# Optimization experiments

Measured on AMD Instinct MI355X. Metric: run time of the kernel, lower is better.

## Reference

```python
import jax, jax.numpy as jnp
import numpy as np

N_NODES = 50000
N_EDGES = 800000
IN_CH = 128
HID_CH = 128
OUT_CH = 64
N_GRAPHS = 256


def setup_inputs() -> dict:
    key = jax.random.key(0)
    k1, k2, k3, k4, k5, k6, k7 = jax.random.split(key, 7)
    x = jax.random.normal(k1, (N_NODES, IN_CH), dtype=jnp.float32)
    edge_index = jax.random.randint(k2, (2, N_EDGES), 0, N_NODES, dtype=jnp.int64)
    batch = jnp.sort(jax.random.randint(k3, (N_NODES,), 0, N_GRAPHS, dtype=jnp.int64))
    # GCNConv params (glorot-ish scale) and Linear params
    W1 = jax.random.normal(k4, (IN_CH, HID_CH), dtype=jnp.float32) / np.sqrt(IN_CH)
    b1 = jnp.zeros((HID_CH,), dtype=jnp.float32)
    W2 = jax.random.normal(k5, (HID_CH, OUT_CH), dtype=jnp.float32) / np.sqrt(HID_CH)
    b2 = jax.random.normal(k6, (OUT_CH,), dtype=jnp.float32) * 0.01
    return {"x": x, "edge_index": edge_index, "batch": batch,
            "W1": W1, "b1": b1, "W2": W2, "b2": b2}


def _gcn_conv(x, edge_index, W, b):
    # PyG GCNConv: add self loops, symmetric normalization, linear transform,
    # gather-scale-scatter aggregation, bias.
    n = x.shape[0]
    loop = jnp.arange(n, dtype=edge_index.dtype)
    src = jnp.concatenate([edge_index[0], loop])  # message sources
    dst = jnp.concatenate([edge_index[1], loop])  # aggregation targets
    deg = jax.ops.segment_sum(jnp.ones_like(dst, dtype=x.dtype), dst, num_segments=n)
    dinv = jnp.where(deg > 0, jax.lax.rsqrt(deg), 0.0)
    norm = dinv[src] * dinv[dst]                  # [E+N]
    h = x @ W                                     # [N, hid] transform first (in >= hid)
    msg = h[src] * norm[:, None]                  # [E+N, hid] gather + scale
    agg = jax.ops.segment_sum(msg, dst, num_segments=n)  # scatter-add
    return agg + b


def reference(x, edge_index, batch, W1, b1, W2, b2):
    h = _gcn_conv(x, edge_index, W1, b1)
    h = jax.nn.relu(h)
    # dropout is identity in eval mode
    pooled = jax.ops.segment_max(h, batch, num_segments=N_GRAPHS)  # global max pool
    pooled = jnp.where(jnp.isfinite(pooled), pooled, 0.0)          # empty graphs -> 0
    out = jax.nn.relu(pooled @ W2 + b2)
    return out
```

## Files before the change

### kernel.cpp

```cpp
#include <hip/hip_runtime.h>

#define NN 50000
#define NE 800000
#define NG 256
#define NB 256
#define BW 196
#define NBIN 200
#define EPB 4000
#define NGEMM 391
#define PAD 16
#define CAP 4608
#define WT_STRIDE 136

typedef __attribute__((ext_vector_type(8))) short bf16x8;
typedef __attribute__((ext_vector_type(4))) float f32x4;
typedef __attribute__((ext_vector_type(2))) float f32x2;

static __device__ __forceinline__ unsigned short f2b(float f) {
    unsigned int u = __float_as_uint(f);
    return (unsigned short)((u + 0x7FFFu + ((u >> 16) & 1u)) >> 16);
}
static __device__ __forceinline__ unsigned char f2e4m3(float f) {
    int p = __builtin_amdgcn_cvt_pk_fp8_f32(f, 0.f, 0, false);
    return (unsigned char)(p & 0xFF);
}

__global__ __launch_bounds__(256) void k_front(const float* __restrict__ x,
                                               const float* __restrict__ W,
                                               unsigned char* __restrict__ h8,
                                               const int* __restrict__ src,
                                               const int* __restrict__ dst,
                                               int* __restrict__ bcur,
                                               unsigned int* __restrict__ ebuf) {
    __shared__ unsigned short Ws[128 * WT_STRIDE];
    const int tid = threadIdx.x;

    if (blockIdx.x >= NGEMM) {
        int* lh = (int*)Ws;
        int* gb = lh + NB;
        int* lc = gb + NB;
        lh[tid] = 0; lc[tid] = 0;
        __syncthreads();
        int e0 = (blockIdx.x - NGEMM) * EPB;
        for (int i = e0 + tid; i < e0 + EPB; i += 256)
            atomicAdd(&lh[(unsigned)dst[i] / BW], 1);
        __syncthreads();
        if (lh[tid]) gb[tid] = tid * CAP + atomicAdd(&bcur[tid * PAD], lh[tid]);
        __syncthreads();
        for (int i = e0 + tid; i < e0 + EPB; i += 256) {
            int d = dst[i];
            int b = (unsigned)d / BW;
            int r = atomicAdd(&lc[b], 1);
            ebuf[gb[b] + r] = ((unsigned)(d - b * BW) << 17) | (unsigned)src[i];
        }
        return;
    }

#pragma unroll
    for (int p = 0; p < 64; ++p) {
        int g = p * 256 + tid;
        int k = g >> 7, n = g & 127;
        Ws[n * WT_STRIDE + k] = f2b(W[g]);
    }
    __syncthreads();
    const int w = tid >> 6, lane = tid & 63;
    const int q = lane >> 4, lid = lane & 15;
    const int m0 = blockIdx.x * 128 + w * 32;
    f32x4 acc[2][8];
#pragma unroll
    for (int rt = 0; rt < 2; ++rt)
#pragma unroll
        for (int jt = 0; jt < 8; ++jt) acc[rt][jt] = (f32x4){0.f, 0.f, 0.f, 0.f};

#pragma unroll
    for (int kt = 0; kt < 4; ++kt) {
        bf16x8 a[2];
#pragma unroll
        for (int rt = 0; rt < 2; ++rt) {
            int m = m0 + rt * 16 + lid;
            int k0 = kt * 32 + q * 8;
            float4 p0 = make_float4(0.f, 0.f, 0.f, 0.f), p1 = p0;
            if (m < NN) {
                p0 = *(const float4*)(x + (size_t)m * 128 + k0);
                p1 = *(const float4*)(x + (size_t)m * 128 + k0 + 4);
            }
            a[rt][0] = (short)f2b(p0.x); a[rt][1] = (short)f2b(p0.y);
            a[rt][2] = (short)f2b(p0.z); a[rt][3] = (short)f2b(p0.w);
            a[rt][4] = (short)f2b(p1.x); a[rt][5] = (short)f2b(p1.y);
            a[rt][6] = (short)f2b(p1.z); a[rt][7] = (short)f2b(p1.w);
        }
#pragma unroll
        for (int jt = 0; jt < 8; ++jt) {
            bf16x8 b = *(const bf16x8*)(Ws + (jt * 16 + lid) * WT_STRIDE + kt * 32 + q * 8);
            acc[0][jt] = __builtin_amdgcn_mfma_f32_16x16x32_bf16(a[0], b, acc[0][jt], 0, 0, 0);
            acc[1][jt] = __builtin_amdgcn_mfma_f32_16x16x32_bf16(a[1], b, acc[1][jt], 0, 0, 0);
        }
    }
#pragma unroll
    for (int rt = 0; rt < 2; ++rt)
#pragma unroll
        for (int reg = 0; reg < 4; ++reg) {
            int gr = m0 + rt * 16 + q * 4 + reg;
            if (gr < NN) {
#pragma unroll
                for (int jt = 0; jt < 8; ++jt)
                    h8[(size_t)gr * 128 + jt * 16 + lid] = f2e4m3(acc[rt][jt][reg]);
            }
        }
}

__global__ __launch_bounds__(256) void k_sort(const unsigned int* __restrict__ ebuf,
                                              const int* __restrict__ bcur,
                                              int* __restrict__ csr_src,
                                              int* __restrict__ rowptr,
                                              int* __restrict__ deg,
                                              float* __restrict__ dinv) {
    __shared__ int hist[NB], off[NB], cur[NB];
    __shared__ int stage[CAP];
    const int t = threadIdx.x;
    const int b = blockIdx.x;
    const int cnt = bcur[b * PAD];
    const int ebeg = b * CAP;
    const int nbase = b * BW;
    hist[t] = 0; cur[t] = 0;
    __syncthreads();
    for (int i = t; i < cnt; i += 256)
        atomicAdd(&hist[ebuf[ebeg + i] >> 17], 1);
    __syncthreads();
    int v = hist[t];
    off[t] = v;
    __syncthreads();
    for (int o = 1; o < NB; o <<= 1) {
        int u = (t >= o) ? off[t - o] : 0;
        __syncthreads();
        off[t] += u;
        __syncthreads();
    }
    int ex = off[t] - v;
    int gn = nbase + t;
    if (t < BW && gn < NN) {
        rowptr[gn] = ebeg + ex;
        deg[gn] = v;
        dinv[gn] = rsqrtf((float)(v + 1));
    }
    __syncthreads();
    off[t] = ex;
    __syncthreads();
    for (int i = t; i < cnt; i += 256) {
        unsigned int p = ebuf[ebeg + i];
        int l = p >> 17;
        int r = atomicAdd(&cur[l], 1);
        stage[off[l] + r] = (int)(p & 0x1FFFFu);
    }
    __syncthreads();
    for (int i = t; i < cnt; i += 256)
        csr_src[ebeg + i] = stage[i];
}

__global__ __launch_bounds__(256) void k_agg(const unsigned char* __restrict__ h8,
                                             const int* __restrict__ csr_src,
                                             const int* __restrict__ rowptr,
                                             const int* __restrict__ deg,
                                             const float* __restrict__ dinv,
                                             const float* __restrict__ b1,
                                             const int* __restrict__ batch,
                                             int* __restrict__ pooled) {
    const int tid = threadIdx.x;
    const int qg = tid >> 4, ql = tid & 15;
    const int n = blockIdx.x * 16 + qg;
    __shared__ float vals[16][128];
    __shared__ int bts[16];
    if (ql == 0) bts[qg] = batch[n];
    const float dd = dinv[n];
    const int beg = rowptr[n];
    const int end = beg + deg[n];
    const int c = ql * 8;
    float a[8];
#pragma unroll
    for (int j = 0; j < 8; ++j) a[j] = 0.f;
#pragma unroll 4
    for (int i = beg; i < end; ++i) {
        int s = csr_src[i];
        float ds = dinv[s];
        uint2 v = *(const uint2*)(h8 + (size_t)s * 128 + c);
        f32x2 f0 = __builtin_amdgcn_cvt_pk_f32_fp8((int)v.x, false);
        f32x2 f1 = __builtin_amdgcn_cvt_pk_f32_fp8((int)v.x, true);
        f32x2 f2 = __builtin_amdgcn_cvt_pk_f32_fp8((int)v.y, false);
        f32x2 f3 = __builtin_amdgcn_cvt_pk_f32_fp8((int)v.y, true);
        a[0] = fmaf(ds, f0.x, a[0]); a[1] = fmaf(ds, f0.y, a[1]);
        a[2] = fmaf(ds, f1.x, a[2]); a[3] = fmaf(ds, f1.y, a[3]);
        a[4] = fmaf(ds, f2.x, a[4]); a[5] = fmaf(ds, f2.y, a[5]);
        a[6] = fmaf(ds, f3.x, a[6]); a[7] = fmaf(ds, f3.y, a[7]);
    }
    {
        uint2 hv = *(const uint2*)(h8 + (size_t)n * 128 + c);
        f32x2 f0 = __builtin_amdgcn_cvt_pk_f32_fp8((int)hv.x, false);
        f32x2 f1 = __builtin_amdgcn_cvt_pk_f32_fp8((int)hv.x, true);
        f32x2 f2 = __builtin_amdgcn_cvt_pk_f32_fp8((int)hv.y, false);
        f32x2 f3 = __builtin_amdgcn_cvt_pk_f32_fp8((int)hv.y, true);
        float4 b0 = *(const float4*)(b1 + c);
        float4 b4 = *(const float4*)(b1 + c + 4);
        float r0 = fmaxf(dd * fmaf(dd, f0.x, a[0]) + b0.x, 0.f);
        float r1 = fmaxf(dd * fmaf(dd, f0.y, a[1]) + b0.y, 0.f);
        float r2 = fmaxf(dd * fmaf(dd, f1.x, a[2]) + b0.z, 0.f);
        float r3 = fmaxf(dd * fmaf(dd, f1.y, a[3]) + b0.w, 0.f);
        float r4 = fmaxf(dd * fmaf(dd, f2.x, a[4]) + b4.x, 0.f);
        float r5 = fmaxf(dd * fmaf(dd, f2.y, a[5]) + b4.y, 0.f);
        float r6 = fmaxf(dd * fmaf(dd, f3.x, a[6]) + b4.z, 0.f);
        float r7 = fmaxf(dd * fmaf(dd, f3.y, a[7]) + b4.w, 0.f);
        *(float4*)&vals[qg][c] = make_float4(r0, r1, r2, r3);
        *(float4*)&vals[qg][c + 4] = make_float4(r4, r5, r6, r7);
    }
    __syncthreads();
    if (tid < 128) {
        float m = vals[0][tid];
        int cur = bts[0];
#pragma unroll
        for (int ww = 1; ww < 16; ++ww) {
            if (bts[ww] != cur) {
                atomicMax(&pooled[cur * 128 + tid], __float_as_int(m));
                cur = bts[ww];
                m = vals[ww][tid];
            } else {
                m = fmaxf(m, vals[ww][tid]);
            }
        }
        atomicMax(&pooled[cur * 128 + tid], __float_as_int(m));
    }
}

__global__ __launch_bounds__(256) void k_gemm2(const float* __restrict__ pooled,
                                               const float* __restrict__ W2,
                                               const float* __restrict__ b2,
                                               float* __restrict__ out) {
    const int tid = threadIdx.x;
    const int row = blockIdx.x * 4 + (tid >> 6);
    const int col = tid & 63;
    const float* p = pooled + row * 128;
    float acc = b2[col];
    for (int k = 0; k < 128; ++k) acc += p[k] * W2[k * 64 + col];
    out[row * 64 + col] = fmaxf(acc, 0.f);
}

extern "C" void kernel_launch(void* const* d_in, const int* in_sizes, int n_in,
                              void* d_out, int out_size, void* d_ws, size_t ws_size,
                              hipStream_t stream) {
    const float* x     = (const float*)d_in[0];
    const int*   ei    = (const int*)d_in[1];
    const int*   batch = (const int*)d_in[2];
    const float* W1    = (const float*)d_in[3];
    const float* b1    = (const float*)d_in[4];
    const float* W2    = (const float*)d_in[5];
    const float* b2    = (const float*)d_in[6];
    float* out = (float*)d_out;

    int*   pooled  = (int*)d_ws;
    int*   bcur    = pooled + (size_t)NG * 128;
    int*   rowptr  = bcur + NB * PAD;
    int*   deg     = rowptr + NN;
    float* dinv    = (float*)(deg + NN);
    int*   csr_src = (int*)(dinv + NN);
    unsigned int* ebuf = (unsigned int*)(csr_src + (size_t)NB * CAP);
    unsigned char* h8  = (unsigned char*)(ebuf + (size_t)NB * CAP);

    size_t zbytes = ((size_t)NG * 128 + NB * PAD) * 4;
    hipMemsetAsync(d_ws, 0, zbytes, stream);

    const int* srcv = ei;
    const int* dstv = ei + NE;

    k_front<<<NGEMM + NBIN, 256, 0, stream>>>(x, W1, h8, srcv, dstv, bcur, ebuf);
    k_sort<<<NB, 256, 0, stream>>>(ebuf, bcur, csr_src, rowptr, deg, dinv);
    k_agg<<<NN / 16, 256, 0, stream>>>(h8, csr_src, rowptr, deg, dinv, b1, batch, pooled);
    k_gemm2<<<NG / 4, 256, 0, stream>>>((const float*)pooled, W2, b2, out);
}
```

Measured before the change: 137.7 us.

## Fuse all four kernels into one persistent kernel with grid barriers

Merges the GEMM/binning, per-bucket sort, aggregation/pooling and final GEMM kernels into a single launch of 768 blocks. The phases are separated by atomic-counter grid barriers, and the aggregation phase becomes a grid-stride loop over node tiles. Zeroing of the pooled buffer moves into the sort phase, which shrinks the host memset. The aim is to remove inter-kernel launch gaps. In exchange it adds barrier spin cost, and it relies on all 768 blocks being co-resident, so it could deadlock if occupancy falls short.

```diff
diff --git a/kernel.cpp b/kernel.cpp
--- a/kernel.cpp
+++ b/kernel.cpp
@@ -8,6 +8,9 @@
 #define NBIN 200
 #define EPB 4000
 #define NGEMM 391
+#define NFRONT (NGEMM + NBIN)
+#define GRID 768
+#define NAGG (NN / 16)
 #define PAD 16
 #define CAP 4608
 #define WT_STRIDE 136
@@ -25,23 +28,91 @@
     return (unsigned char)(p & 0xFF);
 }
 
-__global__ __launch_bounds__(256) void k_front(const float* __restrict__ x,
-                                               const float* __restrict__ W,
-                                               unsigned char* __restrict__ h8,
-                                               const int* __restrict__ src,
-                                               const int* __restrict__ dst,
-                                               int* __restrict__ bcur,
-                                               unsigned int* __restrict__ ebuf) {
-    __shared__ unsigned short Ws[128 * WT_STRIDE];
+static __device__ __forceinline__ void gbar(int* c, int target) {
+    __syncthreads();
+    if (threadIdx.x == 0) {
+        __threadfence();
+        atomicAdd(c, 1);
+        while (atomicAdd(c, 0) < target)
+            __builtin_amdgcn_s_sleep(8);
+        __threadfence();
+    }
+    __syncthreads();
+}
+
+__global__ __launch_bounds__(256, 3) void k_all(
+        const float* __restrict__ x, const float* __restrict__ W,
+        unsigned char* __restrict__ h8,
+        const int* __restrict__ src, const int* __restrict__ dst,
+        int* __restrict__ bcur, unsigned int* __restrict__ ebuf,
+        int* __restrict__ csr_src, int* __restrict__ rowptr,
+        int* __restrict__ deg, float* __restrict__ dinv,
+        const float* __restrict__ b1, const int* __restrict__ batch,
+        int* __restrict__ pooled,
+        const float* __restrict__ W2, const float* __restrict__ b2,
+        float* __restrict__ out, int* __restrict__ bars) {
+    __shared__ __align__(16) unsigned short Ws[128 * WT_STRIDE];
     const int tid = threadIdx.x;
-
-    if (blockIdx.x >= NGEMM) {
+    const int bid = blockIdx.x;
+
+    if (bid < NGEMM) {
+#pragma unroll
+        for (int p = 0; p < 64; ++p) {
+            int g = p * 256 + tid;
+            int k = g >> 7, n = g & 127;
+            Ws[n * WT_STRIDE + k] = f2b(W[g]);
+        }
+        __syncthreads();
+        const int w = tid >> 6, lane = tid & 63;
+        const int q = lane >> 4, lid = lane & 15;
+        const int m0 = bid * 128 + w * 32;
+        f32x4 acc[2][8];
+#pragma unroll
+        for (int rt = 0; rt < 2; ++rt)
+#pragma unroll
+            for (int jt = 0; jt < 8; ++jt) acc[rt][jt] = (f32x4){0.f, 0.f, 0.f, 0.f};
+#pragma unroll
+        for (int kt = 0; kt < 4; ++kt) {
+            bf16x8 a[2];
+#pragma unroll
+            for (int rt = 0; rt < 2; ++rt) {
+                int m = m0 + rt * 16 + lid;
+                int k0 = kt * 32 + q * 8;
+                float4 p0 = make_float4(0.f, 0.f, 0.f, 0.f), p1 = p0;
+                if (m < NN) {
+                    p0 = *(const float4*)(x + (size_t)m * 128 + k0);
+                    p1 = *(const float4*)(x + (size_t)m * 128 + k0 + 4);
+                }
+                a[rt][0] = (short)f2b(p0.x); a[rt][1] = (short)f2b(p0.y);
+                a[rt][2] = (short)f2b(p0.z); a[rt][3] = (short)f2b(p0.w);
+                a[rt][4] = (short)f2b(p1.x); a[rt][5] = (short)f2b(p1.y);
+                a[rt][6] = (short)f2b(p1.z); a[rt][7] = (short)f2b(p1.w);
+            }
+#pragma unroll
+            for (int jt = 0; jt < 8; ++jt) {
+                bf16x8 b = *(const bf16x8*)(Ws + (jt * 16 + lid) * WT_STRIDE + kt * 32 + q * 8);
+                acc[0][jt] = __builtin_amdgcn_mfma_f32_16x16x32_bf16(a[0], b, acc[0][jt], 0, 0, 0);
+                acc[1][jt] = __builtin_amdgcn_mfma_f32_16x16x32_bf16(a[1], b, acc[1][jt], 0, 0, 0);
+            }
+        }
+#pragma unroll
+        for (int rt = 0; rt < 2; ++rt)
+#pragma unroll
+            for (int reg = 0; reg < 4; ++reg) {
+                int gr = m0 + rt * 16 + q * 4 + reg;
+                if (gr < NN) {
+#pragma unroll
+                    for (int jt = 0; jt < 8; ++jt)
+                        h8[(size_t)gr * 128 + jt * 16 + lid] = f2e4m3(acc[rt][jt][reg]);
+                }
+            }
+    } else if (bid < NFRONT) {
         int* lh = (int*)Ws;
         int* gb = lh + NB;
         int* lc = gb + NB;
         lh[tid] = 0; lc[tid] = 0;
         __syncthreads();
-        int e0 = (blockIdx.x - NGEMM) * EPB;
+        int e0 = (bid - NGEMM) * EPB;
         for (int i = e0 + tid; i < e0 + EPB; i += 256)
             atomicAdd(&lh[(unsigned)dst[i] / BW], 1);
         __syncthreads();
@@ -53,193 +124,130 @@
             int r = atomicAdd(&lc[b], 1);
             ebuf[gb[b] + r] = ((unsigned)(d - b * BW) << 17) | (unsigned)src[i];
         }
-        return;
-    }
-
-#pragma unroll
-    for (int p = 0; p < 64; ++p) {
-        int g = p * 256 + tid;
-        int k = g >> 7, n = g & 127;
-        Ws[n * WT_STRIDE + k] = f2b(W[g]);
-    }
-    __syncthreads();
-    const int w = tid >> 6, lane = tid & 63;
-    const int q = lane >> 4, lid = lane & 15;
-    const int m0 = blockIdx.x * 128 + w * 32;
-    f32x4 acc[2][8];
-#pragma unroll
-    for (int rt = 0; rt < 2; ++rt)
-#pragma unroll
-        for (int jt = 0; jt < 8; ++jt) acc[rt][jt] = (f32x4){0.f, 0.f, 0.f, 0.f};
-
-#pragma unroll
-    for (int kt = 0; kt < 4; ++kt) {
-        bf16x8 a[2];
-#pragma unroll
-        for (int rt = 0; rt < 2; ++rt) {
-            int m = m0 + rt * 16 + lid;
-            int k0 = kt * 32 + q * 8;
-            float4 p0 = make_float4(0.f, 0.f, 0.f, 0.f), p1 = p0;
-            if (m < NN) {
-                p0 = *(const float4*)(x + (size_t)m * 128 + k0);
-                p1 = *(const float4*)(x + (size_t)m * 128 + k0 + 4);
-            }
-            a[rt][0] = (short)f2b(p0.x); a[rt][1] = (short)f2b(p0.y);
-            a[rt][2] = (short)f2b(p0.z); a[rt][3] = (short)f2b(p0.w);
-            a[rt][4] = (short)f2b(p1.x); a[rt][5] = (short)f2b(p1.y);
-            a[rt][6] = (short)f2b(p1.z); a[rt][7] = (short)f2b(p1.w);
-        }
-#pragma unroll
-        for (int jt = 0; jt < 8; ++jt) {
-            bf16x8 b = *(const bf16x8*)(Ws + (jt * 16 + lid) * WT_STRIDE + kt * 32 + q * 8);
-            acc[0][jt] = __builtin_amdgcn_mfma_f32_16x16x32_bf16(a[0], b, acc[0][jt], 0, 0, 0);
-            acc[1][jt] = __builtin_amdgcn_mfma_f32_16x16x32_bf16(a[1], b, acc[1][jt], 0, 0, 0);
-        }
-    }
-#pragma unroll
-    for (int rt = 0; rt < 2; ++rt)
-#pragma unroll
-        for (int reg = 0; reg < 4; ++reg) {
-            int gr = m0 + rt * 16 + q * 4 + reg;
-            if (gr < NN) {
-#pragma unroll
-                for (int jt = 0; jt < 8; ++jt)
-                    h8[(size_t)gr * 128 + jt * 16 + lid] = f2e4m3(acc[rt][jt][reg]);
-            }
-        }
-}
-
-__global__ __launch_bounds__(256) void k_sort(const unsigned int* __restrict__ ebuf,
-                                              const int* __restrict__ bcur,
-                                              int* __restrict__ csr_src,
-                                              int* __restrict__ rowptr,
-                                              int* __restrict__ deg,
-                                              float* __restrict__ dinv) {
-    __shared__ int hist[NB], off[NB], cur[NB];
-    __shared__ int stage[CAP];
-    const int t = threadIdx.x;
-    const int b = blockIdx.x;
-    const int cnt = bcur[b * PAD];
-    const int ebeg = b * CAP;
-    const int nbase = b * BW;
-    hist[t] = 0; cur[t] = 0;
-    __syncthreads();
-    for (int i = t; i < cnt; i += 256)
-        atomicAdd(&hist[ebuf[ebeg + i] >> 17], 1);
-    __syncthreads();
-    int v = hist[t];
-    off[t] = v;
-    __syncthreads();
-    for (int o = 1; o < NB; o <<= 1) {
-        int u = (t >= o) ? off[t - o] : 0;
-        __syncthreads();
-        off[t] += u;
-        __syncthreads();
-    }
-    int ex = off[t] - v;
-    int gn = nbase + t;
-    if (t < BW && gn < NN) {
-        rowptr[gn] = ebeg + ex;
-        deg[gn] = v;
-        dinv[gn] = rsqrtf((float)(v + 1));
-    }
-    __syncthreads();
-    off[t] = ex;
-    __syncthreads();
-    for (int i = t; i < cnt; i += 256) {
-        unsigned int p = ebuf[ebeg + i];
-        int l = p >> 17;
-        int r = atomicAdd(&cur[l], 1);
-        stage[off[l] + r] = (int)(p & 0x1FFFFu);
-    }
-    __syncthreads();
-    for (int i = t; i < cnt; i += 256)
-        csr_src[ebeg + i] = stage[i];
-}
-
-__global__ __launch_bounds__(256) void k_agg(const unsigned char* __restrict__ h8,
-                                             const int* __restrict__ csr_src,
-                                             const int* __restrict__ rowptr,
-                                             const int* __restrict__ deg,
-                                             const float* __restrict__ dinv,
-                                             const float* __restrict__ b1,
-                                             const int* __restrict__ batch,
-                                             int* __restrict__ pooled) {
-    const int tid = threadIdx.x;
-    const int qg = tid >> 4, ql = tid & 15;
-    const int n = blockIdx.x * 16 + qg;
-    __shared__ float vals[16][128];
-    __shared__ int bts[16];
-    if (ql == 0) bts[qg] = batch[n];
-    const float dd = dinv[n];
-    const int beg = rowptr[n];
-    const int end = beg + deg[n];
-    const int c = ql * 8;
-    float a[8];
-#pragma unroll
-    for (int j = 0; j < 8; ++j) a[j] = 0.f;
+    }
+    gbar(&bars[0], GRID);
+
+    if (bid < NB) {
+        if (tid < 128) pooled[bid * 128 + tid] = 0;
+        int* hist = (int*)Ws;
+        int* off = hist + NB;
+        int* cur = off + NB;
+        int* stage = cur + NB;
+        const int cnt = bcur[bid * PAD];
+        const int ebeg = bid * CAP;
+        const int nbase = bid * BW;
+        hist[tid] = 0; cur[tid] = 0;
+        __syncthreads();
+        for (int i = tid; i < cnt; i += 256)
+            atomicAdd(&hist[ebuf[ebeg + i] >> 17], 1);
+        __syncthreads();
+        int v = hist[tid];
+        off[tid] = v;
+        __syncthreads();
+        for (int o = 1; o < NB; o <<= 1) {
+            int u = (tid >= o) ? off[tid - o] : 0;
+            __syncthreads();
+            off[tid] += u;
+            __syncthreads();
+        }
+        int ex = off[tid] - v;
+        int gn = nbase + tid;
+        if (tid < BW && gn < NN) {
+            rowptr[gn] = ebeg + ex;
+            deg[gn] = v;
+            dinv[gn] = rsqrtf((float)(v + 1));
+        }
+        __syncthreads();
+        off[tid] = ex;
+        __syncthreads();
+        for (int i = tid; i < cnt; i += 256) {
+            unsigned int p = ebuf[ebeg + i];
+            int l = p >> 17;
+            int r = atomicAdd(&cur[l], 1);
+            stage[off[l] + r] = (int)(p & 0x1FFFFu);
+        }
+        __syncthreads();
+        for (int i = tid; i < cnt; i += 256)
+            csr_src[ebeg + i] = stage[i];
+    }
+    gbar(&bars[1], GRID);
+
+    {
+        float* vals = (float*)Ws;
+        int* bts = (int*)Ws + 2048;
+        const int qg = tid >> 4, ql = tid & 15;
+        const int c = ql * 8;
+        for (int vtile = bid; vtile < NAGG; vtile += GRID) {
+            const int n = vtile * 16 + qg;
+            if (ql == 0) bts[qg] = batch[n];
+            const float dd = dinv[n];
+            const int beg = rowptr[n];
+            const int end = beg + deg[n];
+            float a[8];
+#pragma unroll
+            for (int j = 0; j < 8; ++j) a[j] = 0.f;
 #pragma unroll 4
-    for (int i = beg; i < end; ++i) {
-        int s = csr_src[i];
-        float ds = dinv[s];
-        uint2 v = *(const uint2*)(h8 + (size_t)s * 128 + c);
-        f32x2 f0 = __builtin_amdgcn_cvt_pk_f32_fp8((int)v.x, false);
-        f32x2 f1 = __builtin_amdgcn_cvt_pk_f32_fp8((int)v.x, true);
-        f32x2 f2 = __builtin_amdgcn_cvt_pk_f32_fp8((int)v.y, false);
-        f32x2 f3 = __builtin_amdgcn_cvt_pk_f32_fp8((int)v.y, true);
-        a[0] = fmaf(ds, f0.x, a[0]); a[1] = fmaf(ds, f0.y, a[1]);
-        a[2] = fmaf(ds, f1.x, a[2]); a[3] = fmaf(ds, f1.y, a[3]);
-        a[4] = fmaf(ds, f2.x, a[4]); a[5] = fmaf(ds, f2.y, a[5]);
-        a[6] = fmaf(ds, f3.x, a[6]); a[7] = fmaf(ds, f3.y, a[7]);
-    }
-    {
-        uint2 hv = *(const uint2*)(h8 + (size_t)n * 128 + c);
-        f32x2 f0 = __builtin_amdgcn_cvt_pk_f32_fp8((int)hv.x, false);
-        f32x2 f1 = __builtin_amdgcn_cvt_pk_f32_fp8((int)hv.x, true);
-        f32x2 f2 = __builtin_amdgcn_cvt_pk_f32_fp8((int)hv.y, false);
-        f32x2 f3 = __builtin_amdgcn_cvt_pk_f32_fp8((int)hv.y, true);
-        float4 b0 = *(const float4*)(b1 + c);
-        float4 b4 = *(const float4*)(b1 + c + 4);
-        float r0 = fmaxf(dd * fmaf(dd, f0.x, a[0]) + b0.x, 0.f);
-        float r1 = fmaxf(dd * fmaf(dd, f0.y, a[1]) + b0.y, 0.f);
-        float r2 = fmaxf(dd * fmaf(dd, f1.x, a[2]) + b0.z, 0.f);
-        float r3 = fmaxf(dd * fmaf(dd, f1.y, a[3]) + b0.w, 0.f);
-        float r4 = fmaxf(dd * fmaf(dd, f2.x, a[4]) + b4.x, 0.f);
-        float r5 = fmaxf(dd * fmaf(dd, f2.y, a[5]) + b4.y, 0.f);
-        float r6 = fmaxf(dd * fmaf(dd, f3.x, a[6]) + b4.z, 0.f);
-        float r7 = fmaxf(dd * fmaf(dd, f3.y, a[7]) + b4.w, 0.f);
-        *(float4*)&vals[qg][c] = make_float4(r0, r1, r2, r3);
-        *(float4*)&vals[qg][c + 4] = make_float4(r4, r5, r6, r7);
-    }
-    __syncthreads();
-    if (tid < 128) {
-        float m = vals[0][tid];
-        int cur = bts[0];
-#pragma unroll
-        for (int ww = 1; ww < 16; ++ww) {
-            if (bts[ww] != cur) {
+            for (int i = beg; i < end; ++i) {
+                int s = csr_src[i];
+                float ds = dinv[s];
+                uint2 v = *(const uint2*)(h8 + (size_t)s * 128 + c);
+                f32x2 f0 = __builtin_amdgcn_cvt_pk_f32_fp8((int)v.x, false);
+                f32x2 f1 = __builtin_amdgcn_cvt_pk_f32_fp8((int)v.x, true);
+                f32x2 f2 = __builtin_amdgcn_cvt_pk_f32_fp8((int)v.y, false);
+                f32x2 f3 = __builtin_amdgcn_cvt_pk_f32_fp8((int)v.y, true);
+                a[0] = fmaf(ds, f0.x, a[0]); a[1] = fmaf(ds, f0.y, a[1]);
+                a[2] = fmaf(ds, f1.x, a[2]); a[3] = fmaf(ds, f1.y, a[3]);
+                a[4] = fmaf(ds, f2.x, a[4]); a[5] = fmaf(ds, f2.y, a[5]);
+                a[6] = fmaf(ds, f3.x, a[6]); a[7] = fmaf(ds, f3.y, a[7]);
+            }
+            {
+                uint2 hv = *(const uint2*)(h8 + (size_t)n * 128 + c);
+                f32x2 f0 = __builtin_amdgcn_cvt_pk_f32_fp8((int)hv.x, false);
+                f32x2 f1 = __builtin_amdgcn_cvt_pk_f32_fp8((int)hv.x, true);
+                f32x2 f2 = __builtin_amdgcn_cvt_pk_f32_fp8((int)hv.y, false);
+                f32x2 f3 = __builtin_amdgcn_cvt_pk_f32_fp8((int)hv.y, true);
+                float4 b0 = *(const float4*)(b1 + c);
+                float4 b4 = *(const float4*)(b1 + c + 4);
+                float r0 = fmaxf(dd * fmaf(dd, f0.x, a[0]) + b0.x, 0.f);
+                float r1 = fmaxf(dd * fmaf(dd, f0.y, a[1]) + b0.y, 0.f);
+                float r2 = fmaxf(dd * fmaf(dd, f1.x, a[2]) + b0.z, 0.f);
+                float r3 = fmaxf(dd * fmaf(dd, f1.y, a[3]) + b0.w, 0.f);
+                float r4 = fmaxf(dd * fmaf(dd, f2.x, a[4]) + b4.x, 0.f);
+                float r5 = fmaxf(dd * fmaf(dd, f2.y, a[5]) + b4.y, 0.f);
+                float r6 = fmaxf(dd * fmaf(dd, f3.x, a[6]) + b4.z, 0.f);
+                float r7 = fmaxf(dd * fmaf(dd, f3.y, a[7]) + b4.w, 0.f);
+                *(float4*)&vals[qg * 128 + c] = make_float4(r0, r1, r2, r3);
+                *(float4*)&vals[qg * 128 + c + 4] = make_float4(r4, r5, r6, r7);
+            }
+            __syncthreads();
+            if (tid < 128) {
+                float m = vals[tid];
+                int cur = bts[0];
+#pragma unroll
+                for (int ww = 1; ww < 16; ++ww) {
+                    if (bts[ww] != cur) {
+                        atomicMax(&pooled[cur * 128 + tid], __float_as_int(m));
+                        cur = bts[ww];
+                        m = vals[ww * 128 + tid];
+                    } else {
+                        m = fmaxf(m, vals[ww * 128 + tid]);
+                    }
+                }
                 atomicMax(&pooled[cur * 128 + tid], __float_as_int(m));
-                cur = bts[ww];
-                m = vals[ww][tid];
-            } else {
-                m = fmaxf(m, vals[ww][tid]);
-            }
-        }
-        atomicMax(&pooled[cur * 128 + tid], __float_as_int(m));
-    }
-}
-
-__global__ __launch_bounds__(256) void k_gemm2(const float* __restrict__ pooled,
-                                               const float* __restrict__ W2,
-                                               const float* __restrict__ b2,
-                                               float* __restrict__ out) {
-    const int tid = threadIdx.x;
-    const int row = blockIdx.x * 4 + (tid >> 6);
-    const int col = tid & 63;
-    const float* p = pooled + row * 128;
-    float acc = b2[col];
-    for (int k = 0; k < 128; ++k) acc += p[k] * W2[k * 64 + col];
-    out[row * 64 + col] = fmaxf(acc, 0.f);
+            }
+            __syncthreads();
+        }
+    }
+    gbar(&bars[2], GRID);
+
+    if (bid < NG / 4) {
+        const int row = bid * 4 + (tid >> 6);
+        const int col = tid & 63;
+        const float* p = (const float*)pooled + row * 128;
+        float acc = b2[col];
+        for (int k = 0; k < 128; ++k) acc += p[k] * W2[k * 64 + col];
+        out[row * 64 + col] = fmaxf(acc, 0.f);
+    }
 }
 
 extern "C" void kernel_launch(void* const* d_in, const int* in_sizes, int n_in,
@@ -254,23 +262,23 @@
     const float* b2    = (const float*)d_in[6];
     float* out = (float*)d_out;
 
-    int*   pooled  = (int*)d_ws;
-    int*   bcur    = pooled + (size_t)NG * 128;
-    int*   rowptr  = bcur + NB * PAD;
+    int*   bcur    = (int*)d_ws;
+    int*   bars    = bcur + NB * PAD;
+    int*   pooled  = bars + 48;
+    int*   rowptr  = pooled + (size_t)NG * 128;
     int*   deg     = rowptr + NN;
     float* dinv    = (float*)(deg + NN);
     int*   csr_src = (int*)(dinv + NN);
     unsigned int* ebuf = (unsigned int*)(csr_src + (size_t)NB * CAP);
     unsigned char* h8  = (unsigned char*)(ebuf + (size_t)NB * CAP);
 
-    size_t zbytes = ((size_t)NG * 128 + NB * PAD) * 4;
+    size_t zbytes = ((size_t)NB * PAD + 48) * 4;
     hipMemsetAsync(d_ws, 0, zbytes, stream);
 
     const int* srcv = ei;
     const int* dstv = ei + NE;
 
-    k_front<<<NGEMM + NBIN, 256, 0, stream>>>(x, W1, h8, srcv, dstv, bcur, ebuf);
-    k_sort<<<NB, 256, 0, stream>>>(ebuf, bcur, csr_src, rowptr, deg, dinv);
-    k_agg<<<NN / 16, 256, 0, stream>>>(h8, csr_src, rowptr, deg, dinv, b1, batch, pooled);
-    k_gemm2<<<NG / 4, 256, 0, stream>>>((const float*)pooled, W2, b2, out);
-}
+    k_all<<<GRID, 256, 0, stream>>>(x, W1, h8, srcv, dstv, bcur, ebuf,
+                                    csr_src, rowptr, deg, dinv, b1, batch,
+                                    pooled, W2, b2, out, bars);
+}
```

After: 387.1 us. +181.1%, slower.

## Pre-convert W1 to bf16 and widen aggregation gathers to 16 bytes

Applied to the files above, without the earlier changes.

Adds a small prep kernel that converts and transposes W1 to padded bf16 once. Each GEMM block then copies that bf16 copy into shared memory with direct global-to-LDS loads, instead of every block converting the fp32 weights itself. The aggregation kernel now uses 8 lanes per node with 16-byte fp8 row loads, covering 32 nodes per block. That cuts gather instruction count and raises the bytes fetched per load. The cost is one extra kernel launch, more accumulator registers per thread, and bounds handling for the partial last block.

```diff
diff --git a/kernel.cpp b/kernel.cpp
--- a/kernel.cpp
+++ b/kernel.cpp
@@ -11,6 +11,7 @@
 #define PAD 16
 #define CAP 4608
 #define WT_STRIDE 136
+#define WBYTES (128 * WT_STRIDE * 2)
 
 typedef __attribute__((ext_vector_type(8))) short bf16x8;
 typedef __attribute__((ext_vector_type(4))) float f32x4;
@@ -25,14 +26,21 @@
     return (unsigned char)(p & 0xFF);
 }
 
+__global__ __launch_bounds__(256) void k_prep(const float* __restrict__ W,
+                                              unsigned short* __restrict__ wbf) {
+    int g = blockIdx.x * 256 + threadIdx.x;
+    int k = g & 127, n = g >> 7;
+    wbf[n * WT_STRIDE + k] = f2b(W[k * 128 + n]);
+}
+
 __global__ __launch_bounds__(256) void k_front(const float* __restrict__ x,
-                                               const float* __restrict__ W,
+                                               const unsigned short* __restrict__ wbf,
                                                unsigned char* __restrict__ h8,
                                                const int* __restrict__ src,
                                                const int* __restrict__ dst,
                                                int* __restrict__ bcur,
                                                unsigned int* __restrict__ ebuf) {
-    __shared__ unsigned short Ws[128 * WT_STRIDE];
+    __shared__ __align__(16) unsigned short Ws[128 * WT_STRIDE];
     const int tid = threadIdx.x;
 
     if (blockIdx.x >= NGEMM) {
@@ -56,11 +64,11 @@
         return;
     }
 
-#pragma unroll
-    for (int p = 0; p < 64; ++p) {
-        int g = p * 256 + tid;
-        int k = g >> 7, n = g & 127;
-        Ws[n * WT_STRIDE + k] = f2b(W[g]);
+    {
+        const int w = tid >> 6, lane = tid & 63;
+        for (int o = w * 1024; o < WBYTES; o += 4096)
+            __builtin_amdgcn_global_load_lds(wbf + (o >> 1) + lane * 8,
+                                             Ws + (o >> 1), 16, 0, 0);
     }
     __syncthreads();
     const int w = tid >> 6, lane = tid & 63;
@@ -166,57 +174,82 @@
                                              const int* __restrict__ batch,
                                              int* __restrict__ pooled) {
     const int tid = threadIdx.x;
-    const int qg = tid >> 4, ql = tid & 15;
-    const int n = blockIdx.x * 16 + qg;
-    __shared__ float vals[16][128];
-    __shared__ int bts[16];
-    if (ql == 0) bts[qg] = batch[n];
-    const float dd = dinv[n];
-    const int beg = rowptr[n];
-    const int end = beg + deg[n];
-    const int c = ql * 8;
-    float a[8];
-#pragma unroll
-    for (int j = 0; j < 8; ++j) a[j] = 0.f;
+    const int g = tid >> 3, gl = tid & 7;
+    const int n = blockIdx.x * 32 + g;
+    __shared__ float vals[32][132];
+    __shared__ int bts[32];
+    const bool valid = (n < NN);
+    if (gl == 0 && valid) bts[g] = batch[n];
+    const float dd = valid ? dinv[n] : 0.f;
+    int beg = 0, end = 0;
+    if (valid) { beg = rowptr[n]; end = beg + deg[n]; }
+    const int c = gl * 16;
+    float a[16];
+#pragma unroll
+    for (int j = 0; j < 16; ++j) a[j] = 0.f;
 #pragma unroll 4
     for (int i = beg; i < end; ++i) {
         int s = csr_src[i];
         float ds = dinv[s];
-        uint2 v = *(const uint2*)(h8 + (size_t)s * 128 + c);
+        uint4 v = *(const uint4*)(h8 + (size_t)s * 128 + c);
         f32x2 f0 = __builtin_amdgcn_cvt_pk_f32_fp8((int)v.x, false);
         f32x2 f1 = __builtin_amdgcn_cvt_pk_f32_fp8((int)v.x, true);
         f32x2 f2 = __builtin_amdgcn_cvt_pk_f32_fp8((int)v.y, false);
         f32x2 f3 = __builtin_amdgcn_cvt_pk_f32_fp8((int)v.y, true);
-        a[0] = fmaf(ds, f0.x, a[0]); a[1] = fmaf(ds, f0.y, a[1]);
-        a[2] = fmaf(ds, f1.x, a[2]); a[3] = fmaf(ds, f1.y, a[3]);
-        a[4] = fmaf(ds, f2.x, a[4]); a[5] = fmaf(ds, f2.y, a[5]);
-        a[6] = fmaf(ds, f3.x, a[6]); a[7] = fmaf(ds, f3.y, a[7]);
-    }
-    {
-        uint2 hv = *(const uint2*)(h8 + (size_t)n * 128 + c);
+        f32x2 f4 = __builtin_amdgcn_cvt_pk_f32_fp8((int)v.z, false);
+        f32x2 f5 = __builtin_amdgcn_cvt_pk_f32_fp8((int)v.z, true);
+        f32x2 f6 = __builtin_amdgcn_cvt_pk_f32_fp8((int)v.w, false);
+        f32x2 f7 = __builtin_amdgcn_cvt_pk_f32_fp8((int)v.w, true);
+        a[0]  = fmaf(ds, f0.x, a[0]);  a[1]  = fmaf(ds, f0.y, a[1]);
+        a[2]  = fmaf(ds, f1.x, a[2]);  a[3]  = fmaf(ds, f1.y, a[3]);
+        a[4]  = fmaf(ds, f2.x, a[4]);  a[5]  = fmaf(ds, f2.y, a[5]);
+        a[6]  = fmaf(ds, f3.x, a[6]);  a[7]  = fmaf(ds, f3.y, a[7]);
+        a[8]  = fmaf(ds, f4.x, a[8]);  a[9]  = fmaf(ds, f4.y, a[9]);
+        a[10] = fmaf(ds, f5.x, a[10]); a[11] = fmaf(ds, f5.y, a[11]);
+        a[12] = fmaf(ds, f6.x, a[12]); a[13] = fmaf(ds, f6.y, a[13]);
+        a[14] = fmaf(ds, f7.x, a[14]); a[15] = fmaf(ds, f7.y, a[15]);
+    }
+    if (valid) {
+        uint4 hv = *(const uint4*)(h8 + (size_t)n * 128 + c);
         f32x2 f0 = __builtin_amdgcn_cvt_pk_f32_fp8((int)hv.x, false);
         f32x2 f1 = __builtin_amdgcn_cvt_pk_f32_fp8((int)hv.x, true);
         f32x2 f2 = __builtin_amdgcn_cvt_pk_f32_fp8((int)hv.y, false);
         f32x2 f3 = __builtin_amdgcn_cvt_pk_f32_fp8((int)hv.y, true);
-        float4 b0 = *(const float4*)(b1 + c);
-        float4 b4 = *(const float4*)(b1 + c + 4);
-        float r0 = fmaxf(dd * fmaf(dd, f0.x, a[0]) + b0.x, 0.f);
-        float r1 = fmaxf(dd * fmaf(dd, f0.y, a[1]) + b0.y, 0.f);
-        float r2 = fmaxf(dd * fmaf(dd, f1.x, a[2]) + b0.z, 0.f);
-        float r3 = fmaxf(dd * fmaf(dd, f1.y, a[3]) + b0.w, 0.f);
-        float r4 = fmaxf(dd * fmaf(dd, f2.x, a[4]) + b4.x, 0.f);
-        float r5 = fmaxf(dd * fmaf(dd, f2.y, a[5]) + b4.y, 0.f);
-        float r6 = fmaxf(dd * fmaf(dd, f3.x, a[6]) + b4.z, 0.f);
-        float r7 = fmaxf(dd * fmaf(dd, f3.y, a[7]) + b4.w, 0.f);
-        *(float4*)&vals[qg][c] = make_float4(r0, r1, r2, r3);
-        *(float4*)&vals[qg][c + 4] = make_float4(r4, r5, r6, r7);
+        f32x2 f4 = __builtin_amdgcn_cvt_pk_f32_fp8((int)hv.z, false);
+        f32x2 f5 = __builtin_amdgcn_cvt_pk_f32_fp8((int)hv.z, true);
+        f32x2 f6 = __builtin_amdgcn_cvt_pk_f32_fp8((int)hv.w, false);
+        f32x2 f7 = __builtin_amdgcn_cvt_pk_f32_fp8((int)hv.w, true);
+        float4 b0  = *(const float4*)(b1 + c);
+        float4 b4  = *(const float4*)(b1 + c + 4);
+        float4 b8  = *(const float4*)(b1 + c + 8);
+        float4 b12 = *(const float4*)(b1 + c + 12);
+        float r0  = fmaxf(dd * fmaf(dd, f0.x, a[0])  + b0.x,  0.f);
+        float r1  = fmaxf(dd * fmaf(dd, f0.y, a[1])  + b0.y,  0.f);
+        float r2  = fmaxf(dd * fmaf(dd, f1.x, a[2])  + b0.z,  0.f);
+        float r3  = fmaxf(dd * fmaf(dd, f1.y, a[3])  + b0.w,  0.f);
+        float r4  = fmaxf(dd * fmaf(dd, f2.x, a[4])  + b4.x,  0.f);
+        float r5  = fmaxf(dd * fmaf(dd, f2.y, a[5])  + b4.y,  0.f);
+        float r6  = fmaxf(dd * fmaf(dd, f3.x, a[6])  + b4.z,  0.f);
+        float r7  = fmaxf(dd * fmaf(dd, f3.y, a[7])  + b4.w,  0.f);
+        float r8  = fmaxf(dd * fmaf(dd, f4.x, a[8])  + b8.x,  0.f);
+        float r9  = fmaxf(dd * fmaf(dd, f4.y, a[9])  + b8.y,  0.f);
+        float r10 = fmaxf(dd * fmaf(dd, f5.x, a[10]) + b8.z,  0.f);
+        float r11 = fmaxf(dd * fmaf(dd, f5.y, a[11]) + b8.w,  0.f);
+        float r12 = fmaxf(dd * fmaf(dd, f6.x, a[12]) + b12.x, 0.f);
+        float r13 = fmaxf(dd * fmaf(dd, f6.y, a[13]) + b12.y, 0.f);
+        float r14 = fmaxf(dd * fmaf(dd, f7.x, a[14]) + b12.z, 0.f);
+        float r15 = fmaxf(dd * fmaf(dd, f7.y, a[15]) + b12.w, 0.f);
+        *(float4*)&vals[g][c]      = make_float4(r0, r1, r2, r3);
+        *(float4*)&vals[g][c + 4]  = make_float4(r4, r5, r6, r7);
+        *(float4*)&vals[g][c + 8]  = make_float4(r8, r9, r10, r11);
+        *(float4*)&vals[g][c + 12] = make_float4(r12, r13, r14, r15);
     }
     __syncthreads();
     if (tid < 128) {
+        const int cnt = min(32, NN - blockIdx.x * 32);
         float m = vals[0][tid];
         int cur = bts[0];
-#pragma unroll
-        for (int ww = 1; ww < 16; ++ww) {
+        for (int ww = 1; ww < cnt; ++ww) {
             if (bts[ww] != cur) {
                 atomicMax(&pooled[cur * 128 + tid], __float_as_int(m));
                 cur = bts[ww];
@@ -262,6 +295,7 @@
     int*   csr_src = (int*)(dinv + NN);
     unsigned int* ebuf = (unsigned int*)(csr_src + (size_t)NB * CAP);
     unsigned char* h8  = (unsigned char*)(ebuf + (size_t)NB * CAP);
+    unsigned short* wbf = (unsigned short*)csr_src;
 
     size_t zbytes = ((size_t)NG * 128 + NB * PAD) * 4;
     hipMemsetAsync(d_ws, 0, zbytes, stream);
@@ -269,8 +303,9 @@
     const int* srcv = ei;
     const int* dstv = ei + NE;
 
-    k_front<<<NGEMM + NBIN, 256, 0, stream>>>(x, W1, h8, srcv, dstv, bcur, ebuf);
+    k_prep<<<64, 256, 0, stream>>>(W1, wbf);
+    k_front<<<NGEMM + NBIN, 256, 0, stream>>>(x, wbf, h8, srcv, dstv, bcur, ebuf);
     k_sort<<<NB, 256, 0, stream>>>(ebuf, bcur, csr_src, rowptr, deg, dinv);
-    k_agg<<<NN / 16, 256, 0, stream>>>(h8, csr_src, rowptr, deg, dinv, b1, batch, pooled);
+    k_agg<<<(NN + 31) / 32, 256, 0, stream>>>(h8, csr_src, rowptr, deg, dinv, b1, batch, pooled);
     k_gemm2<<<NG / 4, 256, 0, stream>>>((const float*)pooled, W2, b2, out);
 }
```

After: 145.8 us. +5.9%, slower.

## Prescale transformed features by source dinv via separate degree kernel

Applied to the files above, without the earlier changes.

Adds a small kernel that counts in-degrees with global atomics before the GEMM. The GEMM epilogue then multiplies each row by rsqrt(deg+1) before quantizing to fp8. The aggregation loop no longer needs a per-edge gather of dinv[s] and a multiply, only plain adds. The cost is an extra kernel launch, an extra memset region and 800K global atomics, and fp8 quantization now applies to pre-scaled values. CAP is also reduced, which shrinks the workspace buffers.

```diff
diff --git a/kernel.cpp b/kernel.cpp
--- a/kernel.cpp
+++ b/kernel.cpp
@@ -9,7 +9,7 @@
 #define EPB 4000
 #define NGEMM 391
 #define PAD 16
-#define CAP 4608
+#define CAP 4352
 #define WT_STRIDE 136
 
 typedef __attribute__((ext_vector_type(8))) short bf16x8;
@@ -25,8 +25,16 @@
     return (unsigned char)(p & 0xFF);
 }
 
+__global__ __launch_bounds__(256) void k_deg(const int* __restrict__ dst,
+                                             int* __restrict__ degp) {
+    int i0 = blockIdx.x * 256 + threadIdx.x;
+    for (int i = i0; i < NE; i += 256 * 256)
+        atomicAdd(&degp[dst[i]], 1);
+}
+
 __global__ __launch_bounds__(256) void k_front(const float* __restrict__ x,
                                                const float* __restrict__ W,
+                                               const int* __restrict__ degp,
                                                unsigned char* __restrict__ h8,
                                                const int* __restrict__ src,
                                                const int* __restrict__ dst,
@@ -102,9 +110,10 @@
         for (int reg = 0; reg < 4; ++reg) {
             int gr = m0 + rt * 16 + q * 4 + reg;
             if (gr < NN) {
+                float di = rsqrtf((float)(degp[gr] + 1));
 #pragma unroll
                 for (int jt = 0; jt < 8; ++jt)
-                    h8[(size_t)gr * 128 + jt * 16 + lid] = f2e4m3(acc[rt][jt][reg]);
+                    h8[(size_t)gr * 128 + jt * 16 + lid] = f2e4m3(acc[rt][jt][reg] * di);
             }
         }
 }
@@ -181,16 +190,13 @@
 #pragma unroll 4
     for (int i = beg; i < end; ++i) {
         int s = csr_src[i];
-        float ds = dinv[s];
         uint2 v = *(const uint2*)(h8 + (size_t)s * 128 + c);
         f32x2 f0 = __builtin_amdgcn_cvt_pk_f32_fp8((int)v.x, false);
         f32x2 f1 = __builtin_amdgcn_cvt_pk_f32_fp8((int)v.x, true);
         f32x2 f2 = __builtin_amdgcn_cvt_pk_f32_fp8((int)v.y, false);
         f32x2 f3 = __builtin_amdgcn_cvt_pk_f32_fp8((int)v.y, true);
-        a[0] = fmaf(ds, f0.x, a[0]); a[1] = fmaf(ds, f0.y, a[1]);
-        a[2] = fmaf(ds, f1.x, a[2]); a[3] = fmaf(ds, f1.y, a[3]);
-        a[4] = fmaf(ds, f2.x, a[4]); a[5] = fmaf(ds, f2.y, a[5]);
-        a[6] = fmaf(ds, f3.x, a[6]); a[7] = fmaf(ds, f3.y, a[7]);
+        a[0] += f0.x; a[1] += f0.y; a[2] += f1.x; a[3] += f1.y;
+        a[4] += f2.x; a[5] += f2.y; a[6] += f3.x; a[7] += f3.y;
     }
     {
         uint2 hv = *(const uint2*)(h8 + (size_t)n * 128 + c);
@@ -200,14 +206,14 @@
         f32x2 f3 = __builtin_amdgcn_cvt_pk_f32_fp8((int)hv.y, true);
         float4 b0 = *(const float4*)(b1 + c);
         float4 b4 = *(const float4*)(b1 + c + 4);
-        float r0 = fmaxf(dd * fmaf(dd, f0.x, a[0]) + b0.x, 0.f);
-        float r1 = fmaxf(dd * fmaf(dd, f0.y, a[1]) + b0.y, 0.f);
-        float r2 = fmaxf(dd * fmaf(dd, f1.x, a[2]) + b0.z, 0.f);
-        float r3 = fmaxf(dd * fmaf(dd, f1.y, a[3]) + b0.w, 0.f);
-        float r4 = fmaxf(dd * fmaf(dd, f2.x, a[4]) + b4.x, 0.f);
-        float r5 = fmaxf(dd * fmaf(dd, f2.y, a[5]) + b4.y, 0.f);
-        float r6 = fmaxf(dd * fmaf(dd, f3.x, a[6]) + b4.z, 0.f);
-        float r7 = fmaxf(dd * fmaf(dd, f3.y, a[7]) + b4.w, 0.f);
+        float r0 = fmaxf(dd * (a[0] + f0.x) + b0.x, 0.f);
+        float r1 = fmaxf(dd * (a[1] + f0.y) + b0.y, 0.f);
+        float r2 = fmaxf(dd * (a[2] + f1.x) + b0.z, 0.f);
+        float r3 = fmaxf(dd * (a[3] + f1.y) + b0.w, 0.f);
+        float r4 = fmaxf(dd * (a[4] + f2.x) + b4.x, 0.f);
+        float r5 = fmaxf(dd * (a[5] + f2.y) + b4.y, 0.f);
+        float r6 = fmaxf(dd * (a[6] + f3.x) + b4.z, 0.f);
+        float r7 = fmaxf(dd * (a[7] + f3.y) + b4.w, 0.f);
         *(float4*)&vals[qg][c] = make_float4(r0, r1, r2, r3);
         *(float4*)&vals[qg][c + 4] = make_float4(r4, r5, r6, r7);
     }
@@ -256,20 +262,22 @@
 
     int*   pooled  = (int*)d_ws;
     int*   bcur    = pooled + (size_t)NG * 128;
-    int*   rowptr  = bcur + NB * PAD;
+    int*   degp    = bcur + NB * PAD;
+    int*   rowptr  = degp + NN;
     int*   deg     = rowptr + NN;
     float* dinv    = (float*)(deg + NN);
     int*   csr_src = (int*)(dinv + NN);
     unsigned int* ebuf = (unsigned int*)(csr_src + (size_t)NB * CAP);
     unsigned char* h8  = (unsigned char*)(ebuf + (size_t)NB * CAP);
 
-    size_t zbytes = ((size_t)NG * 128 + NB * PAD) * 4;
+    size_t zbytes = ((size_t)NG * 128 + NB * PAD + NN) * 4;
     hipMemsetAsync(d_ws, 0, zbytes, stream);
 
     const int* srcv = ei;
     const int* dstv = ei + NE;
 
-    k_front<<<NGEMM + NBIN, 256, 0, stream>>>(x, W1, h8, srcv, dstv, bcur, ebuf);
+    k_deg<<<256, 256, 0, stream>>>(dstv, degp);
+    k_front<<<NGEMM + NBIN, 256, 0, stream>>>(x, W1, degp, h8, srcv, dstv, bcur, ebuf);
     k_sort<<<NB, 256, 0, stream>>>(ebuf, bcur, csr_src, rowptr, deg, dinv);
     k_agg<<<NN / 16, 256, 0, stream>>>(h8, csr_src, rowptr, deg, dinv, b1, batch, pooled);
     k_gemm2<<<NG / 4, 256, 0, stream>>>((const float*)pooled, W2, b2, out);
```

New measurement: 172.4 us. 1.25x slower.
